# Performance work log

Hardware: AMD Instinct MI355X
Metric: run time of the kernel (lower is better)

Reference implementation:

```python
import jax, jax.numpy as jnp
import numpy as np

GRID_SIZE = 8
MARGIN = 1.0
NUM_NEG = 4
SOS_NEG = 8
LOSS_LAMBDA = 1.0
IMG_H, IMG_W = 960, 1280  # desc2 is the stride-GRID_SIZE feature map of this image
BIG = 5.0    # fill for radius-masked entries in FOS distance matrix (> max unit-desc dist 2)
HUGE = 1e6   # fill for invalid entries in SOS candidate scores


def _l2n(x, eps=1e-8):
    return x / (jnp.linalg.norm(x, axis=-1, keepdims=True) + eps)


def _pdist(a, b, eps=1e-12):
    # a: B x N x C, b: B x M x C -> B x N x M euclidean distances
    sq = (jnp.sum(a * a, -1)[..., :, None] + jnp.sum(b * b, -1)[..., None, :]
          - 2.0 * jnp.einsum('bnc,bmc->bnm', a, b))
    return jnp.sqrt(jnp.maximum(sq, eps))


def _bilinear(desc, pts):
    # desc: B x C x H x W, pts: B x N x 2 in (y, x) image-pixel coords -> B x N x C
    B, C, H, W = desc.shape
    g = pts / GRID_SIZE - 0.5  # image coords -> feature-grid coords
    gy = jnp.clip(g[..., 0], 0.0, H - 1.0)
    gx = jnp.clip(g[..., 1], 0.0, W - 1.0)
    y0 = jnp.clip(jnp.floor(gy).astype(jnp.int32), 0, H - 2)
    x0 = jnp.clip(jnp.floor(gx).astype(jnp.int32), 0, W - 2)
    wy = (gy - y0)[:, None, :]
    wx = (gx - x0)[:, None, :]
    flat = desc.reshape(B, C, H * W)
    gat = lambda yi, xi: jnp.take_along_axis(flat, (yi * W + xi)[:, None, :], axis=2)
    v00, v01 = gat(y0, x0), gat(y0, x0 + 1)
    v10, v11 = gat(y0 + 1, x0), gat(y0 + 1, x0 + 1)
    out = (v00 * (1 - wy) * (1 - wx) + v01 * (1 - wy) * wx
           + v10 * wy * (1 - wx) + v11 * wy * wx)
    return out.transpose(0, 2, 1)


def _forward(kp1, w_kp1, kp1_desc, desc2, homo12):
    r = 2.0 * GRID_SIZE  # spatial masking radius
    d1 = _l2n(kp1_desc)                       # B x N x C
    w_desc = _l2n(_bilinear(desc2, w_kp1))    # B x N x C interpolated warped descriptors

    # visibility of kp1 under homography homo12 (kp stored as (y, x))
    ones = jnp.ones_like(kp1[..., :1])
    p = jnp.concatenate([kp1[..., 1:2], kp1[..., 0:1], ones], -1)  # (x, y, 1)
    q = jnp.einsum('bij,bnj->bni', homo12, p)
    qx = q[..., 0] / (q[..., 2] + 1e-8)
    qy = q[..., 1] / (q[..., 2] + 1e-8)
    vis = ((qx >= 0) & (qx < IMG_W) & (qy >= 0) & (qy < IMG_H)).astype(d1.dtype)
    denom = jnp.sum(vis) + 1e-8

    # ---- FOS: hard quad triplet with radius masking ----
    pos = jnp.sqrt(jnp.sum((d1 - w_desc) ** 2, -1) + 1e-12)  # B x N
    D = _pdist(d1, w_desc)          # B x N x N cross descriptor distances
    s22 = _pdist(w_kp1, w_kp1)      # B x N x N warped-coordinate distances
    Dm = jnp.where(s22 <= r, BIG, D)  # mask spatial near-positives (incl. diagonal)
    neg1 = -jax.lax.top_k(-Dm, NUM_NEG)[0]                       # hardest negs per row anchor
    neg2 = -jax.lax.top_k(-Dm.transpose(0, 2, 1), NUM_NEG)[0]    # per column anchor
    t1 = jnp.mean(jax.nn.relu(MARGIN + pos[..., None] - neg1), -1)
    t2 = jnp.mean(jax.nn.relu(MARGIN + pos[..., None] - neg2), -1)
    fos = jnp.sum(vis * 0.5 * (t1 + t2)) / denom

    # ---- SOS: radius-masked second-order similarity regularizer ----
    s11 = _pdist(kp1, kp1)
    d11 = _pdist(d1, d1)
    d22 = _pdist(w_desc, w_desc)
    valid = (s11 > r) & (s22 > r)
    score = jnp.where(valid, d11, HUGE)
    nscore, idx = jax.lax.top_k(-score, SOS_NEG)  # sos_neg hardest valid neighbors
    sel_d11 = -nscore
    sel_d22 = jnp.take_along_axis(d22, idx, axis=2)
    diff2 = jnp.where(sel_d11 < HUGE * 0.1, (sel_d11 - sel_d22) ** 2, 0.0)
    sos_i = jnp.sqrt(jnp.sum(diff2, -1) + 1e-12)
    sos = jnp.sum(vis * sos_i) / denom

    return (fos + sos) * LOSS_LAMBDA


def setup_inputs() -> dict:
    key = jax.random.key(0)
    k1, k2, k3, k4, k5 = jax.random.split(key, 5)
    B, N, C, H, W = 2, 4096, 128, 120, 160
    scale = jnp.array([IMG_H - 1.0, IMG_W - 1.0], dtype=jnp.float32)
    kp1 = jax.random.uniform(k1, (B, N, 2), dtype=jnp.float32) * scale
    w_kp1 = jax.random.uniform(k2, (B, N, 2), dtype=jnp.float32) * scale
    kp1_desc = jax.random.normal(k3, (B, N, C), dtype=jnp.float32)
    desc2 = jax.random.normal(k4, (B, C, H, W), dtype=jnp.float32)
    homo12 = (jnp.tile(jnp.eye(3, dtype=jnp.float32), (B, 1, 1))
              + 0.001 * jax.random.normal(k5, (B, 3, 3), dtype=jnp.float32))
    return {'kp1': kp1, 'w_kp1': w_kp1, 'kp1_desc': kp1_desc,
            'desc2': desc2, 'homo12': homo12}


def reference(kp1, w_kp1, kp1_desc, desc2, homo12):
    return _forward(kp1, w_kp1, kp1_desc, desc2, homo12)
```

## Files before the change

### kernel.cpp

```cpp
#include <hip/hip_runtime.h>
#include <hip/hip_fp16.h>
#include <math.h>

#define NPTS 4096
#define CDIM 128
#define FH 120
#define FW 160
#define PIX (FH * FW)

typedef __attribute__((ext_vector_type(8))) short short8_t;
typedef __attribute__((ext_vector_type(4))) float float4_t;
typedef __attribute__((ext_vector_type(2))) unsigned short ushort2_t;

#define OFF_FRAG  0
#define OFF_WDB   1048576
#define OFF_JA    1572864
#define OFF_JB    1605632
#define OFF_POS   1622016
#define OFF_VIS   1630208
#define OFF_ACC   1638400
#define OFF_D2T   2031632
#define OFF_PARTS 2031632
#define OFF_END   4489232

__device__ __forceinline__ unsigned short f2bf(float f) {
  unsigned int u = __float_as_uint(f);
  u = (u + 0x7fffu + ((u >> 16) & 1u)) >> 16;
  return (unsigned short)u;
}

__device__ __forceinline__ float wavesum(float v) {
#pragma unroll
  for (int off = 1; off < 64; off <<= 1) v += __shfl_xor(v, off, 64);
  return v;
}

typedef const __attribute__((address_space(1))) unsigned int gu32_t;
typedef __attribute__((address_space(3))) unsigned int lu32_t;
__device__ __forceinline__ void gl_lds16(const void* g, void* l) {
  __builtin_amdgcn_global_load_lds((gu32_t*)g, (lu32_t*)l, 16, 0, 0);
}

__global__ __launch_bounds__(256) void transpose_desc2(
    const float* __restrict__ d2, unsigned short* __restrict__ out) {
  __shared__ unsigned short tile[64][130];
  const int bp = blockIdx.x;
  const int b = bp / 300;
  const int p0 = (bp - b * 300) * 64;
  const int tid = threadIdx.x;
  const int grp = tid >> 6, lp = tid & 63;
#pragma unroll 4
  for (int r = 0; r < 32; ++r) {
    int c = (r << 2) | grp;
    float v = d2[((size_t)b * CDIM + c) * PIX + p0 + lp];
    tile[lp][c] = __half_as_ushort(__float2half(v));
  }
  __syncthreads();
  unsigned int* ob = (unsigned int*)(out + ((size_t)b * PIX + p0) * CDIM);
#pragma unroll
  for (int i = 0; i < 16; ++i) {
    int u = (i << 8) | tid;
    int p = u >> 6, cc = (u & 63) << 1;
    unsigned int lo = tile[p][cc], hi = tile[p][cc + 1];
    ob[u] = lo | (hi << 16);
  }
}

#define PREP_TAIL() do {                                                        \
  {                                                                             \
    const int T = (p & (NPTS - 1)) >> 4, cRow = p & 15;                         \
    const int kcL = lane >> 4, quadL = (lane >> 2) & 3, jjL = (lane & 3) * 2;   \
    const size_t off = (size_t)(quadL * 16 + cRow) * 8 + jjL;                   \
    const size_t tb = (((size_t)b * 256 + T) * 2) * 4;                          \
    ushort2_t st; st.x = f2bf(d0); st.y = f2bf(d1v);                            \
    ushort2_t sw; sw.x = f2bf(e0); sw.y = f2bf(e1);                             \
    *(ushort2_t*)(frag + (tb + kcL) * 512 + off) = st;                          \
    *(ushort2_t*)(frag + (tb + 4 + kcL) * 512 + off) = sw;                      \
    ushort2_t swr; swr.x = f2bf(e0); swr.y = f2bf(e1);                          \
    *(ushort2_t*)(wdb + (size_t)p * CDIM + c2) = swr;                           \
  }                                                                             \
  float dd0 = d0 - e0, dd1 = d1v - e1;                                          \
  float ssp = wavesum(dd0 * dd0 + dd1 * dd1);                                   \
  if (lane == 0) {                                                              \
    pos[p] = sqrtf(ssp + 1e-12f);                                               \
    float ky = kp1[p * 2 + 0], kx = kp1[p * 2 + 1];                             \
    jA[p] = make_float4(ky, kx, y, x);                                          \
    jb1[p] = -0.5f * n1;                                                        \
    jb2[p] = -0.5f * n2;                                                        \
    const float* h = homo + b * 9;                                              \
    float t0 = h[0] * kx + h[1] * ky + h[2];                                    \
    float t1 = h[3] * kx + h[4] * ky + h[5];                                    \
    float t2 = h[6] * kx + h[7] * ky + h[8];                                    \
    float qx = t0 / (t2 + 1e-8f), qy = t1 / (t2 + 1e-8f);                       \
    vis[p] = (qx >= 0.0f && qx < 1280.0f && qy >= 0.0f && qy < 960.0f)          \
                 ? 1.0f : 0.0f;                                                 \
  }                                                                             \
} while (0)

__global__ __launch_bounds__(256) void prep_t(
    const float* __restrict__ kp1, const float* __restrict__ wkp1,
    const float* __restrict__ desc, const unsigned short* __restrict__ d2t,
    const float* __restrict__ homo,
    unsigned short* __restrict__ frag, unsigned short* __restrict__ wdb,
    float4* __restrict__ jA, float* __restrict__ jb1, float* __restrict__ jb2,
    float* __restrict__ pos, float* __restrict__ vis, float* __restrict__ acc) {
  const int tid = threadIdx.x;
  if (blockIdx.x == 0 && tid < 4) acc[tid] = 0.0f;
  const int p = blockIdx.x * 4 + (tid >> 6);
  const int lane = tid & 63;
  const int b = p >> 12;
  const int c2 = lane * 2;

  float2 v = *(const float2*)(desc + (size_t)p * CDIM + c2);
  float ss = wavesum(v.x * v.x + v.y * v.y);
  float inv = 1.0f / (sqrtf(ss) + 1e-8f);
  float d0 = v.x * inv, d1v = v.y * inv;
  float n1 = ss * inv * inv;

  float y = wkp1[p * 2 + 0], x = wkp1[p * 2 + 1];
  float gy = fminf(fmaxf(y * 0.125f - 0.5f, 0.0f), (float)(FH - 1));
  float gx = fminf(fmaxf(x * 0.125f - 0.5f, 0.0f), (float)(FW - 1));
  int y0 = (int)floorf(gy); y0 = min(max(y0, 0), FH - 2);
  int x0 = (int)floorf(gx); x0 = min(max(x0, 0), FW - 2);
  float wy = gy - (float)y0, wx = gx - (float)x0;
  float w00 = (1 - wy) * (1 - wx), w01 = (1 - wy) * wx;
  float w10 = wy * (1 - wx), w11 = wy * wx;
  const unsigned int* t00 = (const unsigned int*)
      (d2t + ((size_t)b * PIX + y0 * FW + x0) * CDIM) + lane;
  unsigned int u00 = t00[0], u01 = t00[64];
  unsigned int u10 = t00[FW * 64], u11 = t00[FW * 64 + 64];
  float2 f00 = __half22float2(*(const __half2*)&u00);
  float2 f01 = __half22float2(*(const __half2*)&u01);
  float2 f10 = __half22float2(*(const __half2*)&u10);
  float2 f11 = __half22float2(*(const __half2*)&u11);
  float wv0 = f00.x * w00 + f01.x * w01 + f10.x * w10 + f11.x * w11;
  float wv1 = f00.y * w00 + f01.y * w01 + f10.y * w10 + f11.y * w11;
  float ss2 = wavesum(wv0 * wv0 + wv1 * wv1);
  float inv2 = 1.0f / (sqrtf(ss2) + 1e-8f);
  float e0 = wv0 * inv2, e1 = wv1 * inv2;
  float n2 = ss2 * inv2 * inv2;

  PREP_TAIL();
}

__global__ __launch_bounds__(256) void prep_g(
    const float* __restrict__ kp1, const float* __restrict__ wkp1,
    const float* __restrict__ desc, const float* __restrict__ desc2,
    const float* __restrict__ homo,
    unsigned short* __restrict__ frag, unsigned short* __restrict__ wdb,
    float4* __restrict__ jA, float* __restrict__ jb1, float* __restrict__ jb2,
    float* __restrict__ pos, float* __restrict__ vis, float* __restrict__ acc) {
  const int tid = threadIdx.x;
  if (blockIdx.x == 0 && tid < 4) acc[tid] = 0.0f;
  const int p = blockIdx.x * 4 + (tid >> 6);
  const int lane = tid & 63;
  const int b = p >> 12;
  const int c2 = lane * 2;

  float2 v = *(const float2*)(desc + (size_t)p * CDIM + c2);
  float ss = wavesum(v.x * v.x + v.y * v.y);
  float inv = 1.0f / (sqrtf(ss) + 1e-8f);
  float d0 = v.x * inv, d1v = v.y * inv;
  float n1 = ss * inv * inv;

  float y = wkp1[p * 2 + 0], x = wkp1[p * 2 + 1];
  float gy = fminf(fmaxf(y * 0.125f - 0.5f, 0.0f), (float)(FH - 1));
  float gx = fminf(fmaxf(x * 0.125f - 0.5f, 0.0f), (float)(FW - 1));
  int y0 = (int)floorf(gy); y0 = min(max(y0, 0), FH - 2);
  int x0 = (int)floorf(gx); x0 = min(max(x0, 0), FW - 2);
  float wy = gy - (float)y0, wx = gx - (float)x0;
  float w00 = (1 - wy) * (1 - wx), w01 = (1 - wy) * wx;
  float w10 = wy * (1 - wx), w11 = wy * wx;
  const float* q0 = desc2 + ((size_t)b * CDIM + c2) * PIX + y0 * FW + x0;
  const float* q1 = q0 + PIX;
  float wv0 = q0[0] * w00 + q0[1] * w01 + q0[FW] * w10 + q0[FW + 1] * w11;
  float wv1 = q1[0] * w00 + q1[1] * w01 + q1[FW] * w10 + q1[FW + 1] * w11;
  float ss2 = wavesum(wv0 * wv0 + wv1 * wv1);
  float inv2 = 1.0f / (sqrtf(ss2) + 1e-8f);
  float e0 = wv0 * inv2, e1 = wv1 * inv2;
  float n2 = ss2 * inv2 * inv2;

  PREP_TAIL();
}

__device__ __forceinline__ void ins4m(float v, float* L) {
  float p0 = L[0]; L[0] = fmaxf(L[0], v);
  float p1 = L[1]; L[1] = __builtin_amdgcn_fmed3f(p0, L[1], v);
  float p2 = L[2]; L[2] = __builtin_amdgcn_fmed3f(p1, L[2], v);
  L[3] = __builtin_amdgcn_fmed3f(p2, L[3], v);
}
__device__ __forceinline__ void ins6m(float v, float* L) {
  float p0 = L[0]; L[0] = fmaxf(L[0], v);
  float p1 = L[1]; L[1] = __builtin_amdgcn_fmed3f(p0, L[1], v);
  float p2 = L[2]; L[2] = __builtin_amdgcn_fmed3f(p1, L[2], v);
  float p3 = L[3]; L[3] = __builtin_amdgcn_fmed3f(p2, L[3], v);
  float p4 = L[4]; L[4] = __builtin_amdgcn_fmed3f(p3, L[4], v);
  L[5] = __builtin_amdgcn_fmed3f(p4, L[5], v);
}
__device__ __forceinline__ void ins10m(float v, float* L) {
  float p0 = L[0]; L[0] = fmaxf(L[0], v);
  float pk = p0;
#pragma unroll
  for (int k = 1; k < 9; ++k) {
    float cur = L[k];
    L[k] = __builtin_amdgcn_fmed3f(pk, cur, v);
    pk = cur;
  }
  L[9] = __builtin_amdgcn_fmed3f(pk, L[9], v);
}

__device__ __forceinline__ float packkey(float s, int j) {
  return __uint_as_float((__float_as_uint(s) & 0xFFFFF000u) | (unsigned)j);
}

#define TILE_ONE(BUF, J0) do {                                                  \
  const float4 m1 = *(const float4*)(j1b + (J0) + (quad << 2));                 \
  const float4 m2 = *(const float4*)(j2b + (J0) + (quad << 2));                 \
  short8_t Ad[4], Aw[4];                                                        \
  _Pragma("unroll")                                                             \
  for (int kc = 0; kc < 4; ++kc) {                                              \
    Ad[kc] = *(const short8_t*)&(BUF)[kc * 512 + lane * 8];                     \
    Aw[kc] = *(const short8_t*)&(BUF)[(4 + kc) * 512 + lane * 8];               \
  }                                                                             \
  float4_t aD, aDt, a11;                                                        \
  aD[0] = m2.x; aD[1] = m2.y; aD[2] = m2.z; aD[3] = m2.w;                       \
  aDt[0] = m1.x; aDt[1] = m1.y; aDt[2] = m1.z; aDt[3] = m1.w;                   \
  a11 = aDt;                                                                    \
  _Pragma("unroll")                                                             \
  for (int kc = 0; kc < 4; ++kc) {                                              \
    aD  = __builtin_amdgcn_mfma_f32_16x16x32_bf16(Aw[kc], Bd[kc], aD,  0,0,0);  \
    aDt = __builtin_amdgcn_mfma_f32_16x16x32_bf16(Ad[kc], Bw[kc], aDt, 0,0,0);  \
    a11 = __builtin_amdgcn_mfma_f32_16x16x32_bf16(Ad[kc], Bd[kc], a11, 0,0,0);  \
  }                                                                             \
  _Pragma("unroll")                                                             \
  for (int reg = 0; reg < 4; ++reg) {                                           \
    const int jj = (J0) + (quad << 2) + reg;                                    \
    ins4m(packkey(aD[reg], jj), fD);                                            \
    ins4m(packkey(aDt[reg], jj), fDt);                                          \
    ins6m(packkey(a11[reg], jj), fS);                                           \
  }                                                                             \
} while (0)

#define STAGE2(DST, TGLOB) do {                                                  \
  gl_lds16((TGLOB) + ch * 512 + lane * 8, &DST[0][ch * 512]);                    \
  gl_lds16((TGLOB) + (ch + 1) * 512 + lane * 8, &DST[0][(ch + 1) * 512]);        \
  gl_lds16((TGLOB) + 4096 + ch * 512 + lane * 8, &DST[1][ch * 512]);             \
  gl_lds16((TGLOB) + 4096 + (ch + 1) * 512 + lane * 8, &DST[1][(ch + 1) * 512]); \
} while (0)

__global__ __launch_bounds__(256, 4) void loss_main(
    const unsigned short* __restrict__ frag,
    const float* __restrict__ jb1g, const float* __restrict__ jb2g,
    float* __restrict__ parts) {
  __shared__ __align__(16) unsigned short buf[2][2][4096];

  const int tid = threadIdx.x;
  const int bid = blockIdx.x;
  const int combo = ((bid & 7) << 1) | (bid >> 9);
  const int b   = combo >> 3;
  const int seg = combo & 7;
  const int g   = (bid >> 3) & 63;
  const int wave = tid >> 6, lane = tid & 63;
  const int quad = lane >> 4;
  const int base = b * NPTS;
  const int jbase = seg << 9;

  short8_t Bd[4], Bw[4];
  {
    const unsigned short* fb =
        frag + (((size_t)b * 256 + (g * 4 + wave)) * 8) * 512 + (size_t)lane * 8;
#pragma unroll
    for (int kc = 0; kc < 4; ++kc) {
      Bd[kc] = *(const short8_t*)(fb + kc * 512);
      Bw[kc] = *(const short8_t*)(fb + (4 + kc) * 512);
    }
  }

  float fD[4], fDt[4], fS[6];
#pragma unroll
  for (int k = 0; k < 4; ++k) { fD[k] = -1e30f; fDt[k] = -1e30f; }
#pragma unroll
  for (int k = 0; k < 6; ++k) fS[k] = -1e30f;

  const unsigned short* fa = frag + (((size_t)b * 256 + (jbase >> 4)) * 8) * 512;
  const float* j1b = jb1g + base;
  const float* j2b = jb2g + base;
  const int ch = wave << 1;

  STAGE2(buf[0], fa);
  __syncthreads();

  for (int t = 0; t < 32; t += 4) {
    STAGE2(buf[1], fa + 8192);
    TILE_ONE(buf[0][0], jbase + (t << 4));
    TILE_ONE(buf[0][1], jbase + ((t + 1) << 4));
    __syncthreads();
    if (t + 4 < 32) STAGE2(buf[0], fa + 16384);
    TILE_ONE(buf[1][0], jbase + ((t + 2) << 4));
    TILE_ONE(buf[1][1], jbase + ((t + 3) << 4));
    __syncthreads();
    fa += 16384;
  }

  float eD[6], eDt[6], eS[10];
#pragma unroll
  for (int k = 0; k < 4; ++k) { eD[k] = fD[k]; eDt[k] = fDt[k]; }
  eD[4] = eD[5] = eDt[4] = eDt[5] = -1e30f;
#pragma unroll
  for (int k = 0; k < 6; ++k) eS[k] = fS[k];
  eS[6] = eS[7] = eS[8] = eS[9] = -1e30f;

  {
    float tmp[10];
#pragma unroll
    for (int off = 16; off <= 32; off <<= 1) {
#pragma unroll
      for (int k = 0; k < 6; ++k) tmp[k] = eD[k];
#pragma unroll
      for (int k = 0; k < 6; ++k) ins6m(__shfl_xor(tmp[k], off, 64), eD);
#pragma unroll
      for (int k = 0; k < 6; ++k) tmp[k] = eDt[k];
#pragma unroll
      for (int k = 0; k < 6; ++k) ins6m(__shfl_xor(tmp[k], off, 64), eDt);
#pragma unroll
      for (int k = 0; k < 10; ++k) tmp[k] = eS[k];
#pragma unroll
      for (int k = 0; k < 10; ++k) ins10m(__shfl_xor(tmp[k], off, 64), eS);
    }
  }

  if (lane < 16) {
    float* P = parts + (size_t)(seg * 22) * 8192 +
               (base + g * 64 + wave * 16 + lane);
#pragma unroll
    for (int k = 0; k < 6; ++k) {
      P[(size_t)k * 8192] = eD[k];
      P[(size_t)(6 + k) * 8192] = eDt[k];
    }
#pragma unroll
    for (int k = 0; k < 10; ++k) P[(size_t)(12 + k) * 8192] = eS[k];
  }
}

__device__ __forceinline__ float bflo(unsigned int u) { return __uint_as_float(u << 16); }
__device__ __forceinline__ float bfhi(unsigned int u) { return __uint_as_float(u & 0xFFFF0000u); }

__global__ __launch_bounds__(256) void merge_filter(
    const float* __restrict__ parts, const float4* __restrict__ jAg,
    const float* __restrict__ jb1g, const float* __restrict__ jb2g,
    const float* __restrict__ posg,
    const float* __restrict__ visg, const unsigned short* __restrict__ wdb,
    float* __restrict__ accum, float* __restrict__ out) {
  __shared__ int sJ[256];
  __shared__ float sD11[256], sD22[256], sT[64], sVis[32], sN2[32];
  const int tid = threadIdx.x;
  const int a0 = blockIdx.x * 32;

  if (tid < 64) {
    const int al = tid & 31;
    const int type = tid >> 5;
    const int a = a0 + al;
    const int base = a & ~(NPTS - 1);
    float L[6];
#pragma unroll
    for (int k = 0; k < 6; ++k) L[k] = -1e30f;
    const float* P = parts + (size_t)(type * 6) * 8192 + a;
#pragma unroll
    for (int s = 0; s < 8; ++s) {
#pragma unroll
      for (int k = 0; k < 6; ++k) ins6m(P[(size_t)(s * 22 + k) * 8192], L);
    }
    const float4 own = jAg[a];
    const float pv = posg[a];
    const float nsel = -2.0f * (type ? jb2g[a] : jb1g[a]);
    float ts = 0.0f;
    int got = 0;
#pragma unroll
    for (int k = 0; k < 6; ++k) {
      int j = (int)(__float_as_uint(L[k]) & 0xFFFu);
      float4 jc = jAg[base + j];
      float dz = own.z - jc.z, dw = own.w - jc.w;
      if (got < 4 && dz * dz + dw * dw > 256.0f) {
        float d2 = fmaf(-2.0f, L[k], nsel);
        ts += fmaxf(1.0f + pv - sqrtf(fmaxf(d2, 1e-12f)), 0.0f);
        got++;
      }
    }
    sT[tid] = ts;
  } else if (tid < 96) {
    const int al = tid - 64;
    const int a = a0 + al;
    const int base = a & ~(NPTS - 1);
    float S[10];
#pragma unroll
    for (int k = 0; k < 10; ++k) S[k] = -1e30f;
    const float* P = parts + (size_t)12 * 8192 + a;
#pragma unroll
    for (int s = 0; s < 8; ++s) {
#pragma unroll
      for (int k = 0; k < 10; ++k) ins10m(P[(size_t)(s * 22 + k) * 8192], S);
    }
    const float4 own = jAg[a];
    const float n1i = -2.0f * jb1g[a];
    int m = 0;
#pragma unroll
    for (int k = 0; k < 10; ++k) {
      int j = (int)(__float_as_uint(S[k]) & 0xFFFu);
      float4 jc = jAg[base + j];
      float ay = own.x - jc.x, ax = own.y - jc.y;
      float wz = own.z - jc.z, ww = own.w - jc.w;
      if (m < 8 && ay * ay + ax * ax > 256.0f && wz * wz + ww * ww > 256.0f) {
        sJ[al * 8 + m] = base + j;
        sD11[al * 8 + m] = sqrtf(fmaxf(fmaf(-2.0f, S[k], n1i), 1e-12f));
        m++;
      }
    }
    for (int k = m; k < 8; ++k) sJ[al * 8 + k] = -1;
    sVis[al] = visg[a];
    sN2[al] = -2.0f * jb2g[a];
  }
  __syncthreads();

  {
    const int slot = tid;
    const int al = slot >> 3;
    const int j = sJ[slot];
    float d22 = 0.0f;
    if (j >= 0) {
      const uint4* pi = (const uint4*)(wdb + (size_t)(a0 + al) * CDIM);
      const uint4* pj = (const uint4*)(wdb + (size_t)j * CDIM);
      float dot = 0.0f;
#pragma unroll
      for (int qq = 0; qq < 16; ++qq) {
        uint4 ui = pi[qq], uj = pj[qq];
        dot = fmaf(bflo(ui.x), bflo(uj.x), dot); dot = fmaf(bfhi(ui.x), bfhi(uj.x), dot);
        dot = fmaf(bflo(ui.y), bflo(uj.y), dot); dot = fmaf(bfhi(ui.y), bfhi(uj.y), dot);
        dot = fmaf(bflo(ui.z), bflo(uj.z), dot); dot = fmaf(bfhi(ui.z), bfhi(uj.z), dot);
        dot = fmaf(bflo(ui.w), bflo(uj.w), dot); dot = fmaf(bfhi(ui.w), bfhi(uj.w), dot);
      }
      d22 = sqrtf(fmaxf(fmaf(-2.0f, jb2g[j] + dot, sN2[al]), 1e-12f));
    }
    sD22[slot] = d22;
  }
  __syncthreads();

  float contrib = 0.0f, vsum = 0.0f;
  if (tid < 32) {
    float s = 0.0f;
#pragma unroll
    for (int k = 0; k < 8; ++k) {
      if (sJ[tid * 8 + k] >= 0) {
        float d = sD11[tid * 8 + k] - sD22[tid * 8 + k];
        s = fmaf(d, d, s);
      }
    }
    contrib = sVis[tid] * (0.125f * (sT[tid] + sT[32 + tid]) + sqrtf(s + 1e-12f));
    vsum = sVis[tid];
  }
  if (tid < 64) {
#pragma unroll
    for (int off = 32; off >= 1; off >>= 1) {
      contrib += __shfl_down(contrib, off, 64);
      vsum += __shfl_down(vsum, off, 64);
    }
    if (tid == 0) {
      atomicAdd(&accum[0], contrib);
      atomicAdd(&accum[1], vsum);
      __threadfence();
      float old = atomicAdd(&accum[2], 1.0f);
      if (old == 255.0f) {
        float t = atomicAdd(&accum[0], 0.0f);
        float v = atomicAdd(&accum[1], 0.0f);
        out[0] = t / (v + 1e-8f);
      }
    }
  }
}

extern "C" void kernel_launch(void* const* d_in, const int* in_sizes, int n_in,
                              void* d_out, int out_size, void* d_ws, size_t ws_size,
                              hipStream_t stream) {
  (void)in_sizes; (void)n_in; (void)out_size;
  const float* kp1   = (const float*)d_in[0];
  const float* wkp1  = (const float*)d_in[1];
  const float* desc  = (const float*)d_in[2];
  const float* desc2 = (const float*)d_in[3];
  const float* homo  = (const float*)d_in[4];
  float* ws = (float*)d_ws;
  unsigned short* frag = (unsigned short*)(ws + OFF_FRAG);
  unsigned short* wdb  = (unsigned short*)(ws + OFF_WDB);
  float4* jA = (float4*)(ws + OFF_JA);
  float* jb1 = ws + OFF_JB;
  float* jb2 = ws + OFF_JB + 8192;
  float* pos = ws + OFF_POS;
  float* vis = ws + OFF_VIS;
  float* acc = ws + OFF_ACC;
  float* parts = ws + OFF_PARTS;
  unsigned short* d2t = (unsigned short*)(ws + OFF_D2T);

  if (ws_size >= (size_t)OFF_END * 4) {
    transpose_desc2<<<600, 256, 0, stream>>>(desc2, d2t);
    prep_t<<<2048, 256, 0, stream>>>(kp1, wkp1, desc, d2t, homo,
                                     frag, wdb, jA, jb1, jb2, pos, vis, acc);
  } else {
    prep_g<<<2048, 256, 0, stream>>>(kp1, wkp1, desc, desc2, homo,
                                     frag, wdb, jA, jb1, jb2, pos, vis, acc);
  }
  loss_main<<<1024, 256, 0, stream>>>(frag, jb1, jb2, parts);
  merge_filter<<<256, 256, 0, stream>>>(parts, jA, jb1, jb2, pos, vis, wdb, acc,
                                        (float*)d_out);
}
```

Before: 148.5 us.

## Use 4-slot LDS ring with per-tile prefetch and single barrier

Replaces the two-stage double buffer, which staged two tiles and used two full __syncthreads per four tiles, with a 4-slot ring. Each step prefetches the tile two ahead plus the next tile's margin values. Synchronisation uses a vmcnt wait and one s_barrier per tile instead of full syncthreads, and the MFMA block is wrapped in s_setprio to favour matrix issue. The aim is deeper overlap of global-to-LDS loads with compute and hiding the per-tile margin load latency. The risk is that the hand-counted vmcnt values are wrong if the compiler reorders or adds memory ops, and there are more barriers per tile.

```diff
diff --git a/kernel.cpp b/kernel.cpp
--- a/kernel.cpp
+++ b/kernel.cpp
@@ -213,25 +213,25 @@
   return __uint_as_float((__float_as_uint(s) & 0xFFFFF000u) | (unsigned)j);
 }
 
-#define TILE_ONE(BUF, J0) do {                                                  \
-  const float4 m1 = *(const float4*)(j1b + (J0) + (quad << 2));                 \
-  const float4 m2 = *(const float4*)(j2b + (J0) + (quad << 2));                 \
+#define TILE_ONE(BP, J0, M1, M2) do {                                           \
   short8_t Ad[4], Aw[4];                                                        \
   _Pragma("unroll")                                                             \
   for (int kc = 0; kc < 4; ++kc) {                                              \
-    Ad[kc] = *(const short8_t*)&(BUF)[kc * 512 + lane * 8];                     \
-    Aw[kc] = *(const short8_t*)&(BUF)[(4 + kc) * 512 + lane * 8];               \
+    Ad[kc] = *(const short8_t*)((BP) + kc * 512 + lane * 8);                    \
+    Aw[kc] = *(const short8_t*)((BP) + (4 + kc) * 512 + lane * 8);              \
   }                                                                             \
   float4_t aD, aDt, a11;                                                        \
-  aD[0] = m2.x; aD[1] = m2.y; aD[2] = m2.z; aD[3] = m2.w;                       \
-  aDt[0] = m1.x; aDt[1] = m1.y; aDt[2] = m1.z; aDt[3] = m1.w;                   \
+  aD[0] = (M2).x; aD[1] = (M2).y; aD[2] = (M2).z; aD[3] = (M2).w;               \
+  aDt[0] = (M1).x; aDt[1] = (M1).y; aDt[2] = (M1).z; aDt[3] = (M1).w;           \
   a11 = aDt;                                                                    \
+  __builtin_amdgcn_s_setprio(1);                                                \
   _Pragma("unroll")                                                             \
   for (int kc = 0; kc < 4; ++kc) {                                              \
     aD  = __builtin_amdgcn_mfma_f32_16x16x32_bf16(Aw[kc], Bd[kc], aD,  0,0,0);  \
     aDt = __builtin_amdgcn_mfma_f32_16x16x32_bf16(Ad[kc], Bw[kc], aDt, 0,0,0);  \
     a11 = __builtin_amdgcn_mfma_f32_16x16x32_bf16(Ad[kc], Bd[kc], a11, 0,0,0);  \
   }                                                                             \
+  __builtin_amdgcn_s_setprio(0);                                                \
   _Pragma("unroll")                                                             \
   for (int reg = 0; reg < 4; ++reg) {                                           \
     const int jj = (J0) + (quad << 2) + reg;                                    \
@@ -241,18 +241,16 @@
   }                                                                             \
 } while (0)
 
-#define STAGE2(DST, TGLOB) do {                                                  \
-  gl_lds16((TGLOB) + ch * 512 + lane * 8, &DST[0][ch * 512]);                    \
-  gl_lds16((TGLOB) + (ch + 1) * 512 + lane * 8, &DST[0][(ch + 1) * 512]);        \
-  gl_lds16((TGLOB) + 4096 + ch * 512 + lane * 8, &DST[1][ch * 512]);             \
-  gl_lds16((TGLOB) + 4096 + (ch + 1) * 512 + lane * 8, &DST[1][(ch + 1) * 512]); \
+#define STAGE_T(BI, TG) do {                                                    \
+  gl_lds16((TG) + ch * 512 + lane * 8, &buf[BI][ch * 512]);                     \
+  gl_lds16((TG) + (ch + 1) * 512 + lane * 8, &buf[BI][(ch + 1) * 512]);         \
 } while (0)
 
 __global__ __launch_bounds__(256, 4) void loss_main(
     const unsigned short* __restrict__ frag,
     const float* __restrict__ jb1g, const float* __restrict__ jb2g,
     float* __restrict__ parts) {
-  __shared__ __align__(16) unsigned short buf[2][2][4096];
+  __shared__ __align__(16) unsigned short buf[4][4096];
 
   const int tid = threadIdx.x;
   const int bid = blockIdx.x;
@@ -287,19 +285,37 @@
   const float* j2b = jb2g + base;
   const int ch = wave << 1;
 
-  STAGE2(buf[0], fa);
-  __syncthreads();
-
-  for (int t = 0; t < 32; t += 4) {
-    STAGE2(buf[1], fa + 8192);
-    TILE_ONE(buf[0][0], jbase + (t << 4));
-    TILE_ONE(buf[0][1], jbase + ((t + 1) << 4));
-    __syncthreads();
-    if (t + 4 < 32) STAGE2(buf[0], fa + 16384);
-    TILE_ONE(buf[1][0], jbase + ((t + 2) << 4));
-    TILE_ONE(buf[1][1], jbase + ((t + 3) << 4));
-    __syncthreads();
-    fa += 16384;
+  STAGE_T(0, fa);
+  STAGE_T(1, fa + 4096);
+  float4 m1c = *(const float4*)(j1b + jbase + (quad << 2));
+  float4 m2c = *(const float4*)(j2b + jbase + (quad << 2));
+
+  for (int t = 0; t < 30; ++t) {
+    STAGE_T((t + 2) & 3, fa + (size_t)(t + 2) * 4096);
+    const int jn = jbase + ((t + 1) << 4) + (quad << 2);
+    float4 m1n = *(const float4*)(j1b + jn);
+    float4 m2n = *(const float4*)(j2b + jn);
+    asm volatile("s_waitcnt vmcnt(4)" ::: "memory");
+    __builtin_amdgcn_s_barrier();
+    asm volatile("" ::: "memory");
+    TILE_ONE(&buf[t & 3][0], jbase + (t << 4), m1c, m2c);
+    m1c = m1n; m2c = m2n;
+  }
+  {
+    const int jn = jbase + (31 << 4) + (quad << 2);
+    float4 m1n = *(const float4*)(j1b + jn);
+    float4 m2n = *(const float4*)(j2b + jn);
+    asm volatile("s_waitcnt vmcnt(2)" ::: "memory");
+    __builtin_amdgcn_s_barrier();
+    asm volatile("" ::: "memory");
+    TILE_ONE(&buf[30 & 3][0], jbase + (30 << 4), m1c, m2c);
+    m1c = m1n; m2c = m2n;
+  }
+  {
+    asm volatile("s_waitcnt vmcnt(0)" ::: "memory");
+    __builtin_amdgcn_s_barrier();
+    asm volatile("" ::: "memory");
+    TILE_ONE(&buf[31 & 3][0], jbase + (31 << 4), m1c, m2c);
   }
 
   float eD[6], eDt[6], eS[10];
```

New measurement: 149.6 us. Within noise of the previous version (+0.7%).
